# Optimization experiments

Measured on AMD Instinct MI355X. Metric: run time of the kernel, lower is better.

Reference implementation:

```python
import jax, jax.numpy as jnp
from jax import lax
import numpy as np

B, N, XS, LAT = 16, 400000, 256, 10


def setup_inputs() -> dict:
    key = jax.random.key(0)
    ks = jax.random.split(key, 9)
    flow = 2.0 * jax.random.normal(ks[0], (B, N, 3), jnp.float32)
    x = jax.random.normal(ks[1], (B, XS, XS), jnp.float32)
    values = jax.random.normal(ks[2], (N,), jnp.float32)
    # near-identity rotation matrices so most splatted points stay in-grid
    rotations = jnp.eye(3, dtype=jnp.float32)[None] + 0.05 * jax.random.normal(ks[3], (B, 3, 3), jnp.float32)
    shifts = 2.0 * jax.random.normal(ks[4], (B, 2), jnp.float32)
    w1 = 0.001 * jax.random.normal(ks[5], (XS * XS, LAT), jnp.float32)
    b1 = jnp.zeros((LAT,), jnp.float32)
    w2 = 0.1 * jax.random.normal(ks[6], (LAT, 2), jnp.float32)
    b2 = jnp.zeros((2,), jnp.float32)
    inds = jax.random.randint(ks[7], (N, 3), 0, XS, dtype=jnp.int32)
    return dict(flow=flow, x=x, values=values, rotations=rotations, shifts=shifts,
                w1=w1, b1=b1, w2=w2, b2=b2, inds=inds, xsize=XS)


def _gaussian_blur3(imgs):
    # dm_pix.gaussian_blur(sigma=1.0, kernel_size=3): separable, SAME (zero) padding
    g = jnp.exp(jnp.asarray(-0.5, imgs.dtype))
    k = jnp.stack([g, jnp.asarray(1.0, imgs.dtype), g])
    k = k / k.sum()
    xi = imgs[:, None]  # (B,1,H,W)
    kh = k.reshape(1, 1, 3, 1)
    kw = k.reshape(1, 1, 1, 3)
    xi = lax.conv_general_dilated(xi, kh, (1, 1), 'SAME')
    xi = lax.conv_general_dilated(xi, kw, (1, 1), 'SAME')
    return xi[:, 0]


def reference(flow, x, values, rotations, shifts, w1, b1, w2, b2, inds, xsize):
    factor = 0.5 * xsize
    # (1,N,3) coords in (z->x order as in source), center, deform
    coords = jnp.stack([inds[:, 2], inds[:, 1], inds[:, 0]], axis=1)[None].astype(flow.dtype)
    coords = coords - factor + flow                       # (B,N,3)
    coords = jnp.einsum('bnc,brc->bnr', coords, rotations)  # coords @ R^T
    coords = coords[..., :2] - shifts[:, None, :] + factor  # (B,N,2)
    c_sampling = jnp.stack([coords[..., 1], coords[..., 0]], axis=2)  # swap -> (row, col)

    bamp = values[None, :]                                # (1,N) broadcast over B
    bposf = jnp.floor(c_sampling)
    bposi = bposf.astype(jnp.int32)                       # (B,N,2)
    frac = c_sampling - bposf                             # fractional parts
    f0, f1 = frac[:, :, 0], frac[:, :, 1]
    a0 = bamp * (1.0 - f0) * (1.0 - f1)
    a1 = bamp * f0 * (1.0 - f1)
    a2 = bamp * f0 * f1
    a3 = bamp * (1.0 - f0) * f1
    bamp_all = jnp.concatenate([a0, a1, a2, a3], axis=1)  # (B,4N)
    bposi_all = jnp.concatenate([bposi,
                                 bposi + jnp.array((1, 0), jnp.int32),
                                 bposi + jnp.array((1, 1), jnp.int32),
                                 bposi + jnp.array((0, 1), jnp.int32)], axis=1)  # (B,4N,2)

    images = jnp.zeros((flow.shape[0], xsize, xsize), flow.dtype)

    def scatter_img(image, pos_i, amp_i):
        return image.at[pos_i[:, 0], pos_i[:, 1]].add(amp_i)

    images = jax.vmap(scatter_img)(images, bposi_all, bamp_all)
    images = _gaussian_blur3(images)

    # ImageAdjustment: per-image scalar gain/offset from conditioning image x
    h = jax.nn.relu(x.reshape(x.shape[0], -1) @ w1 + b1)
    ab = h @ w2 + b2                                      # (B,2)
    a, b = ab[:, 0], ab[:, 1]
    images = a[:, None, None] * images + b[:, None, None]
    # ctf_type == 'none' -> ctfFilter skipped
    return images
```

## Files before the change

kernel.cpp:

```cpp
#include <hip/hip_runtime.h>

#define XS     256
#define XS2    65536
#define LAT    10
#define BR     8
#define NG     (XS / BR)
#define NBINS  512
#define P1     2048
#define K_MAX  16
#define BINCAP 15360
#define SPLIT  2
#define CELLW  128
#define QS     256.0f
#define INVQS  (1.0f / 256.0f)

__device__ __forceinline__ void lds_add_u64(unsigned long long* p,
                                            unsigned long long v) {
    __hip_atomic_fetch_add(p, v, __ATOMIC_RELAXED, __HIP_MEMORY_SCOPE_WORKGROUP);
}

__device__ __forceinline__ unsigned long long pack4(int q0, int q1, int q2, int q3) {
    return (unsigned long long)((long long)q0 + ((long long)q1 << 16) +
                                ((long long)q2 << 32) + ((long long)q3 << 48));
}

__device__ __forceinline__ void compute_rc(const float* __restrict__ flow,
                                           const int* __restrict__ inds,
                                           const float* __restrict__ rot,
                                           const float* __restrict__ shifts,
                                           int b, int n, int N,
                                           int& r, int& c, float& f0, float& f1) {
    const float* R = rot + b * 9;
    float r00 = R[0], r01 = R[1], r02 = R[2];
    float r10 = R[3], r11 = R[4], r12 = R[5];
    float s0 = shifts[b * 2 + 0], s1 = shifts[b * 2 + 1];
    size_t fo = ((size_t)b * N + n) * 3;
    float fw0 = flow[fo + 0], fw1 = flow[fo + 1], fw2 = flow[fo + 2];
    float v0 = (float)inds[n * 3 + 2] - 128.0f + fw0;
    float v1 = (float)inds[n * 3 + 1] - 128.0f + fw1;
    float v2 = (float)inds[n * 3 + 0] - 128.0f + fw2;
    float p0 = fmaf(v0, r00, fmaf(v1, r01, fmaf(v2, r02, 128.0f - s0)));
    float p1 = fmaf(v0, r10, fmaf(v1, r11, fmaf(v2, r12, 128.0f - s1)));
    float cs0 = p1, cs1 = p0;
    float ff0 = floorf(cs0), ff1 = floorf(cs1);
    r = (int)ff0; c = (int)ff1;
    f0 = cs0 - ff0; f1 = cs1 - ff1;
}

__device__ __forceinline__ void corner_q(int* __restrict__ Q, int rr, int cc, float a) {
    if (rr >= -XS && rr < XS && cc >= -XS && cc < XS) {
        int q = __float2int_rn(a * QS);
        if (q) atomicAdd(&Q[((rr + XS) & (XS - 1)) * XS + ((cc + XS) & (XS - 1))], q);
    }
}

__device__ __forceinline__ bool is_fast(int r) {
    return (r >= -XS) && (r <= XS - 2) && (r != -1);
}

__device__ __forceinline__ void rec_fallback_q(unsigned long long rec, int bin,
                                               int* __restrict__ qimg) {
    unsigned w = (unsigned)rec;
    float amp = __uint_as_float((unsigned)(rec >> 32));
    int b = bin >> 5, g = bin & 31;
    int rig = w & 7, wc = (w >> 3) & 255;
    int wr = g * BR + rig;
    float f0 = (float)((w >> 13) & 511) * (1.0f / 512.0f);
    float f1 = (float)((w >> 22) & 511) * (1.0f / 512.0f);
    float g0 = 1.0f - f0, g1 = 1.0f - f1;
    int* Q = qimg + (size_t)b * XS2;
    if (w & (1u << 11)) {
        int q00 = __float2int_rn(amp * g0 * g1 * QS);
        int q10 = __float2int_rn(amp * f0 * g1 * QS);
        if (q00) atomicAdd(&Q[wr * XS + wc], q00);
        if (q10) atomicAdd(&Q[(wr + 1) * XS + wc], q10);
    }
    if (w & (1u << 12)) {
        int wc1 = (wc + 1) & 255;
        int q01 = __float2int_rn(amp * g0 * f1 * QS);
        int q11 = __float2int_rn(amp * f0 * f1 * QS);
        if (q01) atomicAdd(&Q[wr * XS + wc1], q01);
        if (q11) atomicAdd(&Q[(wr + 1) * XS + wc1], q11);
    }
}

__global__ void init_kernel(uint4* __restrict__ p, int n4) {
    int i = blockIdx.x * blockDim.x + threadIdx.x;
    int stride = gridDim.x * blockDim.x;
    uint4 z; z.x = 0u; z.y = 0u; z.z = 0u; z.w = 0u;
    for (; i < n4; i += stride) p[i] = z;
}

__device__ __forceinline__ void mlp_block(const float* __restrict__ x,
                                          const float* __restrict__ w1,
                                          float* __restrict__ hraw, int id) {
    int t = threadIdx.x;
    int b = id / LAT, l = id - b * LAT;
    const float* xb = x + (size_t)b * XS2;
    float acc = 0.0f;
#pragma unroll 8
    for (int j = 0; j < 256; j++) {
        int e = j * 256 + t;
        acc += xb[e] * w1[(size_t)e * LAT + l];
    }
#pragma unroll
    for (int off = 32; off > 0; off >>= 1) acc += __shfl_down(acc, off);
    __shared__ float red[4];
    if ((t & 63) == 0) red[t >> 6] = acc;
    __syncthreads();
    if (t == 0) hraw[b * LAT + l] = (red[0] + red[1]) + (red[2] + red[3]);
}

__global__ void __launch_bounds__(256)
place_kernel(const float* __restrict__ flow,
             const float* __restrict__ values,
             const int* __restrict__ inds,
             const float* __restrict__ rot,
             const float* __restrict__ shifts,
             const float* __restrict__ x,
             const float* __restrict__ w1,
             float* __restrict__ hraw,
             unsigned* __restrict__ gcursor,
             unsigned long long* __restrict__ recs,
             int* __restrict__ qimg,
             int N, int TI, int IPB, int B) {
    int t = threadIdx.x;

    if (blockIdx.x >= P1) {
        mlp_block(x, w1, hraw, blockIdx.x - P1);
        return;
    }

    __shared__ unsigned lcnt[NBINS];
    __shared__ unsigned lbase[NBINS];
    lcnt[t] = 0; lcnt[t + 256] = 0;
    __syncthreads();

    unsigned long long rec[K_MAX];
    unsigned meta[K_MAX];
    int s = blockIdx.x * IPB;
    int e = min(s + IPB, TI);

#pragma unroll
    for (int k = 0; k < K_MAX; k++) {
        meta[k] = 0xFFFFFFFFu;
        int i = s + t + k * 256;
        if (i < e) {
            int b = i / N, n = i - b * N;
            int r, c; float f0, f1;
            compute_rc(flow, inds, rot, shifts, b, n, N, r, c, f0, f1);
            float amp = values[n];
            if (is_fast(r)) {
                int wr = (r + XS) & (XS - 1);
                int wc = c & (XS - 1);
                unsigned cv0 = (c >= -XS && c < XS) ? 1u : 0u;
                unsigned cv1 = (c + 1 >= -XS && c + 1 < XS) ? 1u : 0u;
                unsigned q0 = min(511u, (unsigned)(f0 * 512.0f + 0.5f));
                unsigned q1 = min(511u, (unsigned)(f1 * 512.0f + 0.5f));
                unsigned word = (unsigned)(wr & 7) | ((unsigned)wc << 3) |
                                (cv0 << 11) | (cv1 << 12) | (q0 << 13) | (q1 << 22);
                int bin = b * NG + (wr >> 3);
                unsigned rank = atomicAdd(&lcnt[bin], 1u);
                meta[k] = (unsigned)bin | (rank << 9);
                rec[k] = ((unsigned long long)__float_as_uint(amp) << 32) | word;
            } else {
                float g0 = 1.0f - f0, g1 = 1.0f - f1;
                int* Q = qimg + (size_t)b * XS2;
                corner_q(Q, r,     c,     amp * g0 * g1);
                corner_q(Q, r + 1, c,     amp * f0 * g1);
                corner_q(Q, r + 1, c + 1, amp * f0 * f1);
                corner_q(Q, r,     c + 1, amp * g0 * f1);
            }
        }
    }
    __syncthreads();

    for (int bin = t; bin < NBINS; bin += 256) {
        unsigned cn = lcnt[bin];
        lbase[bin] = cn ? atomicAdd(&gcursor[bin], cn) : 0u;
    }
    __syncthreads();

#pragma unroll
    for (int k = 0; k < K_MAX; k++) {
        unsigned m = meta[k];
        if (m != 0xFFFFFFFFu) {
            unsigned bin = m & (NBINS - 1);
            unsigned idx = lbase[bin] + (m >> 9);
            if (idx < BINCAP) recs[(size_t)bin * BINCAP + idx] = rec[k];
            else rec_fallback_q(rec[k], (int)bin, qimg);
        }
    }
}

__global__ void __launch_bounds__(256)
accum_kernel(const unsigned long long* __restrict__ recs,
             const unsigned* __restrict__ gcursor,
             float* __restrict__ reps,
             float* __restrict__ aprons, int B) {
    int bin = blockIdx.x >> 1, sp = blockIdx.x & 1;
    int b = bin >> 5, g = bin & 31;
    __shared__ unsigned long long teven[BR * CELLW];
    __shared__ unsigned long long todd[BR * CELLW];
    int t = threadIdx.x;
    for (int k = t; k < BR * CELLW; k += 256) { teven[k] = 0ull; todd[k] = 0ull; }
    __syncthreads();

    unsigned cnt = min(gcursor[bin], (unsigned)BINCAP);
    unsigned lo = (unsigned)(((unsigned long long)cnt * sp) / SPLIT);
    unsigned hi = (unsigned)(((unsigned long long)cnt * (sp + 1)) / SPLIT);
    const unsigned long long* rb = recs + (size_t)bin * BINCAP;

    for (unsigned i = lo + t; i < hi; i += 256) {
        unsigned long long rc = rb[i];
        unsigned w = (unsigned)rc;
        float amp = __uint_as_float((unsigned)(rc >> 32));
        int rig = w & 7, wc = (w >> 3) & 255;
        float f0 = (float)((w >> 13) & 511) * (1.0f / 512.0f);
        float f1 = (float)((w >> 22) & 511) * (1.0f / 512.0f);
        float g0 = 1.0f - f0, g1 = 1.0f - f1;
        bool cv0 = (w >> 11) & 1, cv1 = (w >> 12) & 1;
        int q00 = cv0 ? __float2int_rn(amp * g0 * g1 * QS) : 0;
        int q10 = cv0 ? __float2int_rn(amp * f0 * g1 * QS) : 0;
        int q01 = cv1 ? __float2int_rn(amp * g0 * f1 * QS) : 0;
        int q11 = cv1 ? __float2int_rn(amp * f0 * f1 * QS) : 0;
        unsigned long long inc = pack4(q00, q10, q01, q11);
        unsigned long long* tile = (wc & 1) ? todd : teven;
        lds_add_u64(&tile[rig * CELLW + (wc >> 1)], inc);
    }
    __syncthreads();

    int c = t;
    int je = c >> 1;
    int jo = (c & 1) ? (c >> 1) : (((c + 254) & 255) >> 1);
    bool e_lo = (c & 1) == 0;
    bool o_lo = (c & 1) == 1;
    float* rep = reps + ((size_t)sp * B + b) * XS2;
    float carry = 0.0f;
#pragma unroll
    for (int rig = 0; rig < BR; rig++) {
        long long se = (long long)teven[rig * CELLW + je];
        int e0 = (int)(short)(se & 0xffff); se = (se - e0) >> 16;
        int e1 = (int)(short)(se & 0xffff); se = (se - e1) >> 16;
        int e2 = (int)(short)(se & 0xffff); se = (se - e2) >> 16;
        int e3 = (int)se;
        long long so = (long long)todd[rig * CELLW + jo];
        int o0 = (int)(short)(so & 0xffff); so = (so - o0) >> 16;
        int o1 = (int)(short)(so & 0xffff); so = (so - o1) >> 16;
        int o2 = (int)(short)(so & 0xffff); so = (so - o2) >> 16;
        int o3 = (int)so;
        float r0 = (e_lo ? (float)e0 : (float)e2) + (o_lo ? (float)o0 : (float)o2);
        float r1 = (e_lo ? (float)e1 : (float)e3) + (o_lo ? (float)o1 : (float)o3);
        rep[(g * BR + rig) * XS + c] = (carry + r0) * INVQS;
        carry = r1;
    }
    aprons[((size_t)bin * 2 + sp) * XS + c] = carry * INVQS;
}

__global__ void scatter_kernel(const float* __restrict__ flow,
                               const float* __restrict__ values,
                               const int* __restrict__ inds,
                               const float* __restrict__ rot,
                               const float* __restrict__ shifts,
                               int* __restrict__ qimg, int N) {
    int b = blockIdx.y;
    int n = blockIdx.x * blockDim.x + threadIdx.x;
    if (n >= N) return;
    int r, c; float f0, f1;
    compute_rc(flow, inds, rot, shifts, b, n, N, r, c, f0, f1);
    float amp = values[n];
    float g0 = 1.0f - f0, g1 = 1.0f - f1;
    int* Q = qimg + (size_t)b * XS2;
    corner_q(Q, r,     c,     amp * g0 * g1);
    corner_q(Q, r + 1, c,     amp * f0 * g1);
    corner_q(Q, r + 1, c + 1, amp * f0 * f1);
    corner_q(Q, r,     c + 1, amp * g0 * f1);
}

__global__ void mlp_kernel(const float* __restrict__ x,
                           const float* __restrict__ w1,
                           float* __restrict__ hraw) {
    mlp_block(x, w1, hraw, blockIdx.x);
}

__device__ __forceinline__ float S_load(const int* __restrict__ qimg,
                                        const float* __restrict__ reps,
                                        const float* __restrict__ aprons,
                                        int B, int b, int row, int c, int fast) {
    size_t o = (size_t)b * XS2 + row * XS + c;
    float v = (float)qimg[o] * INVQS;
    if (fast) {
        v += reps[o] + reps[(size_t)B * XS2 + o];
        if (row > 0 && (row & 7) == 0) {
            size_t bin = (size_t)b * NG + ((row >> 3) - 1);
            v += aprons[bin * 2 * XS + c] + aprons[(bin * 2 + 1) * XS + c];
        }
    }
    return v;
}

__global__ void blur_kernel(const int* __restrict__ qimg,
                            const float* __restrict__ reps,
                            const float* __restrict__ aprons,
                            const float* __restrict__ hraw,
                            const float* __restrict__ b1,
                            const float* __restrict__ w2,
                            const float* __restrict__ b2,
                            float* __restrict__ out, int B, int fast) {
    int b = blockIdx.y, r = blockIdx.x, c = threadIdx.x;
    float av = b2[0], bv = b2[1];
#pragma unroll
    for (int l = 0; l < LAT; l++) {
        float h = hraw[b * LAT + l] + b1[l];
        h = h > 0.0f ? h : 0.0f;
        av += h * w2[l * 2 + 0];
        bv += h * w2[l * 2 + 1];
    }
    const float g   = 0.6065306597126334f;
    const float inv = 1.0f / (1.0f + 2.0f * g);
    float up  = (r > 0)      ? S_load(qimg, reps, aprons, B, b, r - 1, c, fast) : 0.0f;
    float mid =                S_load(qimg, reps, aprons, B, b, r,     c, fast);
    float dn  = (r < XS - 1) ? S_load(qimg, reps, aprons, B, b, r + 1, c, fast) : 0.0f;
    float v = (g * (up + dn) + mid) * inv;
    __shared__ float row[XS + 2];
    row[c + 1] = v;
    if (c == 0) { row[0] = 0.0f; row[XS + 1] = 0.0f; }
    __syncthreads();
    float hh = (g * (row[c] + row[c + 2]) + v) * inv;
    out[(size_t)b * XS2 + (size_t)r * XS + c] = av * hh + bv;
}

extern "C" void kernel_launch(void* const* d_in, const int* in_sizes, int n_in,
                              void* d_out, int out_size, void* d_ws, size_t ws_size,
                              hipStream_t stream) {
    const float* flow   = (const float*)d_in[0];
    const float* x      = (const float*)d_in[1];
    const float* values = (const float*)d_in[2];
    const float* rot    = (const float*)d_in[3];
    const float* shifts = (const float*)d_in[4];
    const float* w1     = (const float*)d_in[5];
    const float* b1     = (const float*)d_in[6];
    const float* w2     = (const float*)d_in[7];
    const float* b2     = (const float*)d_in[8];
    const int*   inds   = (const int*)d_in[9];

    int N = in_sizes[2];
    int B = in_sizes[4] / 2;
    int TI  = B * N;
    int IPB = (TI + P1 - 1) / P1;

    size_t imgElems = (size_t)B * XS2;
    int*      qimg    = (int*)d_ws;
    float*    hraw    = (float*)(qimg + imgElems);
    unsigned* gcursor = (unsigned*)(hraw + 256);
    unsigned long long* recs = (unsigned long long*)(gcursor + NBINS);
    float*    reps    = (float*)(recs + (size_t)NBINS * BINCAP);
    float*    aprons  = reps + 2 * imgElems;
    size_t needed = (size_t)((char*)(aprons + (size_t)NBINS * 2 * XS) - (char*)d_ws);

    bool fast = (B * NG == NBINS) && (ws_size >= needed) && (IPB <= K_MAX * 256);

    int n4 = (int)((imgElems * sizeof(int) + 1024 + NBINS * 4) / 16);
    init_kernel<<<512, 256, 0, stream>>>((uint4*)d_ws, n4);

    if (fast) {
        place_kernel<<<P1 + B * LAT, 256, 0, stream>>>(flow, values, inds, rot, shifts,
                                                       x, w1, hraw, gcursor, recs, qimg,
                                                       N, TI, IPB, B);
        accum_kernel<<<NBINS * SPLIT, 256, 0, stream>>>(recs, gcursor, reps, aprons, B);
    } else {
        dim3 g1((N + 255) / 256, B);
        scatter_kernel<<<g1, 256, 0, stream>>>(flow, values, inds, rot, shifts, qimg, N);
        mlp_kernel<<<B * LAT, 256, 0, stream>>>(x, w1, hraw);
    }

    dim3 g3(XS, B);
    blur_kernel<<<g3, qimg ? dim3(XS) : dim3(XS), 0, stream>>>(qimg, reps, aprons, hraw, b1, w2, b2,
                                                               (float*)d_out, B, fast ? 1 : 0);
}
```

Before: 239.2 us.

## Replace register-held records with two-pass recompute in place kernel

The place kernel no longer keeps up to 16 packed records and metadata per thread in registers between the count and write phases. A first pass computes only the row to count bins, and a second pass recomputes the full coordinates and claims slots with a shared-memory atomic on the bin base. This cuts register pressure and raises occupancy, at the cost of reading flow a second time and extra arithmetic. Record order within a bin becomes nondeterministic, and the K_MAX limit on the fast path is dropped.

Measured after the change: 250.9 us. +4.9%, slower.

```diff
diff --git a/kernel.cpp b/kernel.cpp
--- a/kernel.cpp
+++ b/kernel.cpp
@@ -7,7 +7,6 @@
 #define NG     (XS / BR)
 #define NBINS  512
 #define P1     2048
-#define K_MAX  16
 #define BINCAP 15360
 #define SPLIT  2
 #define CELLW  128
@@ -47,6 +46,23 @@
     f0 = cs0 - ff0; f1 = cs1 - ff1;
 }
 
+__device__ __forceinline__ int compute_r(const float* __restrict__ flow,
+                                         const int* __restrict__ inds,
+                                         const float* __restrict__ rot,
+                                         const float* __restrict__ shifts,
+                                         int b, int n, int N) {
+    const float* R = rot + b * 9;
+    float r10 = R[3], r11 = R[4], r12 = R[5];
+    float s1 = shifts[b * 2 + 1];
+    size_t fo = ((size_t)b * N + n) * 3;
+    float fw0 = flow[fo + 0], fw1 = flow[fo + 1], fw2 = flow[fo + 2];
+    float v0 = (float)inds[n * 3 + 2] - 128.0f + fw0;
+    float v1 = (float)inds[n * 3 + 1] - 128.0f + fw1;
+    float v2 = (float)inds[n * 3 + 0] - 128.0f + fw2;
+    float p1 = fmaf(v0, r10, fmaf(v1, r11, fmaf(v2, r12, 128.0f - s1)));
+    return (int)floorf(p1);
+}
+
 __device__ __forceinline__ void corner_q(int* __restrict__ Q, int rr, int cc, float a) {
     if (rr >= -XS && rr < XS && cc >= -XS && cc < XS) {
         int q = __float2int_rn(a * QS);
@@ -136,41 +152,28 @@
     lcnt[t] = 0; lcnt[t + 256] = 0;
     __syncthreads();
 
-    unsigned long long rec[K_MAX];
-    unsigned meta[K_MAX];
     int s = blockIdx.x * IPB;
     int e = min(s + IPB, TI);
-
-#pragma unroll
-    for (int k = 0; k < K_MAX; k++) {
-        meta[k] = 0xFFFFFFFFu;
-        int i = s + t + k * 256;
-        if (i < e) {
-            int b = i / N, n = i - b * N;
-            int r, c; float f0, f1;
-            compute_rc(flow, inds, rot, shifts, b, n, N, r, c, f0, f1);
+    int b0 = s / N;
+    int bBound = (b0 + 1) * N;
+
+    for (int i = s + t; i < e; i += 256) {
+        int b = (i < bBound) ? b0 : b0 + 1;
+        int n = i - b * N;
+        int r = compute_r(flow, inds, rot, shifts, b, n, N);
+        if (is_fast(r)) {
+            int bin = b * NG + (((r + XS) & (XS - 1)) >> 3);
+            atomicAdd(&lcnt[bin], 1u);
+        } else {
+            int rr, c; float f0, f1;
+            compute_rc(flow, inds, rot, shifts, b, n, N, rr, c, f0, f1);
             float amp = values[n];
-            if (is_fast(r)) {
-                int wr = (r + XS) & (XS - 1);
-                int wc = c & (XS - 1);
-                unsigned cv0 = (c >= -XS && c < XS) ? 1u : 0u;
-                unsigned cv1 = (c + 1 >= -XS && c + 1 < XS) ? 1u : 0u;
-                unsigned q0 = min(511u, (unsigned)(f0 * 512.0f + 0.5f));
-                unsigned q1 = min(511u, (unsigned)(f1 * 512.0f + 0.5f));
-                unsigned word = (unsigned)(wr & 7) | ((unsigned)wc << 3) |
-                                (cv0 << 11) | (cv1 << 12) | (q0 << 13) | (q1 << 22);
-                int bin = b * NG + (wr >> 3);
-                unsigned rank = atomicAdd(&lcnt[bin], 1u);
-                meta[k] = (unsigned)bin | (rank << 9);
-                rec[k] = ((unsigned long long)__float_as_uint(amp) << 32) | word;
-            } else {
-                float g0 = 1.0f - f0, g1 = 1.0f - f1;
-                int* Q = qimg + (size_t)b * XS2;
-                corner_q(Q, r,     c,     amp * g0 * g1);
-                corner_q(Q, r + 1, c,     amp * f0 * g1);
-                corner_q(Q, r + 1, c + 1, amp * f0 * f1);
-                corner_q(Q, r,     c + 1, amp * g0 * f1);
-            }
+            float g0 = 1.0f - f0, g1 = 1.0f - f1;
+            int* Q = qimg + (size_t)b * XS2;
+            corner_q(Q, rr,     c,     amp * g0 * g1);
+            corner_q(Q, rr + 1, c,     amp * f0 * g1);
+            corner_q(Q, rr + 1, c + 1, amp * f0 * f1);
+            corner_q(Q, rr,     c + 1, amp * g0 * f1);
         }
     }
     __syncthreads();
@@ -181,15 +184,27 @@
     }
     __syncthreads();
 
-#pragma unroll
-    for (int k = 0; k < K_MAX; k++) {
-        unsigned m = meta[k];
-        if (m != 0xFFFFFFFFu) {
-            unsigned bin = m & (NBINS - 1);
-            unsigned idx = lbase[bin] + (m >> 9);
-            if (idx < BINCAP) recs[(size_t)bin * BINCAP + idx] = rec[k];
-            else rec_fallback_q(rec[k], (int)bin, qimg);
-        }
+    for (int i = s + t; i < e; i += 256) {
+        int b = (i < bBound) ? b0 : b0 + 1;
+        int n = i - b * N;
+        int r, c; float f0, f1;
+        compute_rc(flow, inds, rot, shifts, b, n, N, r, c, f0, f1);
+        if (!is_fast(r)) continue;
+        float amp = values[n];
+        int wr = (r + XS) & (XS - 1);
+        int wc = c & (XS - 1);
+        unsigned cv0 = (c >= -XS && c < XS) ? 1u : 0u;
+        unsigned cv1 = (c + 1 >= -XS && c + 1 < XS) ? 1u : 0u;
+        unsigned q0 = min(511u, (unsigned)(f0 * 512.0f + 0.5f));
+        unsigned q1 = min(511u, (unsigned)(f1 * 512.0f + 0.5f));
+        unsigned word = (unsigned)(wr & 7) | ((unsigned)wc << 3) |
+                        (cv0 << 11) | (cv1 << 12) | (q0 << 13) | (q1 << 22);
+        int bin = b * NG + (wr >> 3);
+        unsigned long long rec =
+            ((unsigned long long)__float_as_uint(amp) << 32) | word;
+        unsigned idx = atomicAdd(&lbase[bin], 1u);
+        if (idx < BINCAP) recs[(size_t)bin * BINCAP + idx] = rec;
+        else rec_fallback_q(rec, bin, qimg);
     }
 }
 
@@ -358,7 +373,7 @@
     float*    aprons  = reps + 2 * imgElems;
     size_t needed = (size_t)((char*)(aprons + (size_t)NBINS * 2 * XS) - (char*)d_ws);
 
-    bool fast = (B * NG == NBINS) && (ws_size >= needed) && (IPB <= K_MAX * 256);
+    bool fast = (B * NG == NBINS) && (ws_size >= needed);
 
     int n4 = (int)((imgElems * sizeof(int) + 1024 + NBINS * 4) / 16);
     init_kernel<<<512, 256, 0, stream>>>((uint4*)d_ws, n4);
@@ -375,6 +390,6 @@
     }
 
     dim3 g3(XS, B);
-    blur_kernel<<<g3, qimg ? dim3(XS) : dim3(XS), 0, stream>>>(qimg, reps, aprons, hraw, b1, w2, b2,
-                                                               (float*)d_out, B, fast ? 1 : 0);
-}
+    blur_kernel<<<g3, XS, 0, stream>>>(qimg, reps, aprons, hraw, b1, w2, b2,
+                                       (float*)d_out, B, fast ? 1 : 0);
+}
```
